# Kernel optimization log

Measured on AMD Instinct MI355X. Metric: run time of the kernel, lower is better.

Reference implementation:

```python
import jax, jax.numpy as jnp
import numpy as np
import math

B, H, S, D = 2, 16, 2048, 128
COEFF = 2.0  # layer_number


def setup_inputs() -> dict:
    key = jax.random.key(0)
    kq, kk, kv = jax.random.split(key, 3)
    return {
        "query_layer": jax.random.normal(kq, (B, H, S, D), dtype=jnp.float32),
        "key_layer": jax.random.normal(kk, (B, H, S, D), dtype=jnp.float32),
        "value_layer": jax.random.normal(kv, (B, H, S, D), dtype=jnp.float32),
    }


def reference(query_layer, key_layer, value_layer):
    b, h, sq, d = query_layer.shape
    sk = key_layer.shape[2]
    norm_factor = math.sqrt(d) * COEFF
    # raw scores [b,h,sq,sk]; divide by sqrt(d)*coeff, cast fp32, multiply by coeff
    scores = jnp.einsum("bhqd,bhkd->bhqk", query_layer, key_layer) / norm_factor
    scores = scores.astype(jnp.float32) * COEFF
    # causal mask (sq == sk path with attention_mask=None)
    causal = jnp.tril(jnp.ones((sq, sk), dtype=bool))
    scores = jnp.where(causal, scores, jnp.float32(-jnp.inf))
    probs = jax.nn.softmax(scores, axis=-1).astype(value_layer.dtype)
    # dropout p=0.0 -> identity
    ctx = jnp.einsum("bhqk,bhkd->bhqd", probs, value_layer)
    # [b,h,sq,d] -> [b,sq,h*d]
    return ctx.transpose(0, 2, 1, 3).reshape(b, sq, h * d)
```

## Files before the change

### kernel.cpp

```cpp
#include <hip/hip_runtime.h>
#include <hip/hip_bf16.h>
#include <math.h>

#define NB 2
#define NH 16
#define NS 2048
#define ND 128

typedef __bf16 bf16x8 __attribute__((ext_vector_type(8)));
typedef __bf16 bf16x4 __attribute__((ext_vector_type(4)));
typedef float f32x4 __attribute__((ext_vector_type(4)));

__global__ __launch_bounds__(256)
void prep(const float* __restrict__ K, const float* __restrict__ V,
          char* __restrict__ Kb, char* __restrict__ Vb)
{
    int g = blockIdx.x * 256 + threadIdx.x;
    if (g < (1 << 20)) {
        const int c8 = g & 15;
        const int row = g >> 4;
        const int s = row & 2047, bh = row >> 11;
        const int jt = s >> 6, r = s & 63;
        const float* src = K + ((size_t)row << 7) + (c8 << 3);
        float4 a = *(const float4*)src;
        float4 c = *(const float4*)(src + 4);
        bf16x8 o;
        o[0]=(__bf16)a.x; o[1]=(__bf16)a.y; o[2]=(__bf16)a.z; o[3]=(__bf16)a.w;
        o[4]=(__bf16)c.x; o[5]=(__bf16)c.y; o[6]=(__bf16)c.z; o[7]=(__bf16)c.w;
        *(bf16x8*)(Kb + (((size_t)(bh*32 + jt)) << 14) + r*256 + ((c8 ^ (r & 7)) << 4)) = o;
    } else {
        g -= (1 << 20);
        const int t   = g >> 10;
        const int off = g & 1023;
        const int d = off >> 3, sl = off & 7;
        const int g8 = sl ^ (d & 7);
        const int bh = t >> 5, jt = t & 31;
        const float* src = V + (((size_t)(bh*2048 + jt*64 + g8*8)) << 7) + d;
        bf16x8 o;
        #pragma unroll
        for (int j = 0; j < 8; ++j) o[j] = (__bf16)src[(size_t)j << 7];
        *(bf16x8*)(Vb + (((size_t)t) << 14) + d*128 + (sl << 4)) = o;
    }
}

__device__ __forceinline__ void gld16(void* lds, const void* gsrc)
{
    __builtin_amdgcn_global_load_lds(
        (const __attribute__((address_space(1))) void*)gsrc,
        (__attribute__((address_space(3))) void*)lds, 16, 0, 0);
}

__global__ __launch_bounds__(256, 2)
void fa_fwd(const float* __restrict__ Qg_, const char* __restrict__ Kb,
            const char* __restrict__ Vb, float* __restrict__ Out)
{
    __shared__ __bf16 Kl[2][8192];
    __shared__ __bf16 Vl[2][8192];
    __shared__ __bf16 Pl[4][1024];

    const int tid  = threadIdx.x;
    const int w    = tid >> 6;
    const int lane = tid & 63;
    const int quad = lane >> 4;
    const int l15  = lane & 15;

    const int pr = blockIdx.x >> 5;
    const int bh = blockIdx.x & 31;
    const int b  = bh >> 4, h = bh & 15;
    const int qtA = 31 - pr, qtB = pr;
    const int ntA = qtA + 1;
    const int total = ntA + qtB + 1;
    const int qA = qtA * 64, qB = qtB * 64;

    const float* Qg = Qg_ + (size_t)bh * NS * ND;
    const char*  Kt = Kb + ((size_t)bh << 19);
    const char*  Vt = Vb + ((size_t)bh << 19);

    const int xo = (l15 & 7) << 4;

    const float CSC = 0.08838834764831845f * 1.4426950408889634f;
    bf16x8 qfA[4], qfB[4], qcur[4];
    {
        const float* qp  = Qg + (size_t)(qA + 16*w + l15) * ND + quad*8;
        const float* qp2 = Qg + (size_t)(qB + 16*w + l15) * ND + quad*8;
        #pragma unroll
        for (int ks = 0; ks < 4; ++ks) {
            float4 a = *(const float4*)(qp + ks*32);
            float4 c = *(const float4*)(qp + ks*32 + 4);
            bf16x8 f;
            f[0]=(__bf16)(a.x*CSC); f[1]=(__bf16)(a.y*CSC); f[2]=(__bf16)(a.z*CSC); f[3]=(__bf16)(a.w*CSC);
            f[4]=(__bf16)(c.x*CSC); f[5]=(__bf16)(c.y*CSC); f[6]=(__bf16)(c.z*CSC); f[7]=(__bf16)(c.w*CSC);
            qfA[ks] = f;
            float4 a2 = *(const float4*)(qp2 + ks*32);
            float4 c2 = *(const float4*)(qp2 + ks*32 + 4);
            bf16x8 f2;
            f2[0]=(__bf16)(a2.x*CSC); f2[1]=(__bf16)(a2.y*CSC); f2[2]=(__bf16)(a2.z*CSC); f2[3]=(__bf16)(a2.w*CSC);
            f2[4]=(__bf16)(c2.x*CSC); f2[5]=(__bf16)(c2.y*CSC); f2[6]=(__bf16)(c2.z*CSC); f2[7]=(__bf16)(c2.w*CSC);
            qfB[ks] = f2;
        }
    }
    #pragma unroll
    for (int ks = 0; ks < 4; ++ks) qcur[ks] = qfA[ks];

    f32x4 O[8];
    #pragma unroll
    for (int dt = 0; dt < 8; ++dt)
        #pragma unroll
        for (int r = 0; r < 4; ++r) O[dt][r] = 0.0f;
    float rs = 0.0f;

    char* const klds0 = (char*)&Kl[0][0];
    char* const vlds0 = (char*)&Vl[0][0];
    char* const Pw    = (char*)&Pl[w][0];

    auto stage = [&](int jt, int buf) {
        const char* kg = Kt + (((size_t)jt) << 14) + w*4096 + lane*16;
        const char* vg = Vt + (((size_t)jt) << 14) + w*4096 + lane*16;
        char* kl = klds0 + buf*16384 + w*4096;
        char* vl = vlds0 + buf*16384 + w*4096;
        #pragma unroll
        for (int i = 0; i < 4; ++i) {
            gld16(kl + i*1024, kg + i*1024);
            gld16(vl + i*1024, vg + i*1024);
        }
    };

    auto flush = [&](int qb) {
        float s1 = rs + __shfl_xor(rs, 16, 64);
        float s2 = s1 + __shfl_xor(s1, 32, 64);
        #pragma unroll
        for (int r = 0; r < 4; ++r) {
            float lsum = __shfl(s2, quad*4 + r, 64);
            float inv = 1.0f / lsum;
            int q = qb + 16*w + quad*4 + r;
            float* op = Out + ((size_t)(b*NS + q)) * (NH*ND) + h*ND + l15;
            #pragma unroll
            for (int dt = 0; dt < 8; ++dt)
                op[dt*16] = O[dt][r] * inv;
        }
    };

    stage(0, 0);
    int cur = 0;

    for (int t = 0; t < total; ++t) {
        const int phase = (t >= ntA);
        const bool diag = (phase ? (t - ntA) == qtB : t == qtA);

        if (t + 1 < total) {
            const int jt2 = (t + 1 >= ntA) ? (t + 1 - ntA) : (t + 1);
            stage(jt2, cur ^ 1);
            asm volatile("s_waitcnt vmcnt(8)" ::: "memory");
        } else {
            asm volatile("s_waitcnt vmcnt(0)" ::: "memory");
        }
        __builtin_amdgcn_s_barrier();
        asm volatile("" ::: "memory");

        if (t == ntA) {
            flush(qA);
            rs = 0.0f;
            #pragma unroll
            for (int dt = 0; dt < 8; ++dt)
                #pragma unroll
                for (int r = 0; r < 4; ++r) O[dt][r] = 0.0f;
            #pragma unroll
            for (int ks = 0; ks < 4; ++ks) qcur[ks] = qfB[ks];
        }

        const char* Kc = klds0 + cur*16384;
        f32x4 Sf[4];
        #pragma unroll
        for (int n = 0; n < 4; ++n)
            #pragma unroll
            for (int r = 0; r < 4; ++r) Sf[n][r] = 0.0f;
        #pragma unroll
        for (int ks = 0; ks < 4; ++ks) {
            bf16x8 kf[4];
            #pragma unroll
            for (int n = 0; n < 4; ++n)
                kf[n] = *(const bf16x8*)(Kc + (n*16 + l15)*256 + ((((ks*4 + quad) << 4)) ^ xo));
            #pragma unroll
            for (int n = 0; n < 4; ++n)
                Sf[n] = __builtin_amdgcn_mfma_f32_16x16x32_bf16(kf[n], qcur[ks], Sf[n], 0, 0, 0);
        }

        #pragma unroll
        for (int n = 0; n < 4; ++n) {
            bf16x4 pk;
            #pragma unroll
            for (int r = 0; r < 4; ++r) {
                float e = exp2f(Sf[n][r]);
                if (diag) {
                    int kvg = n*16 + quad*4 + r;
                    int qg  = 16*w + l15;
                    if (kvg > qg) e = 0.0f;
                }
                pk[r] = (__bf16)e;
                rs += (float)pk[r];
            }
            *(bf16x4*)(Pw + l15*128 + ((((n*2 + (quad >> 1)) << 4)) ^ xo) + ((quad & 1) << 3)) = pk;
        }

        const char* Vc = vlds0 + cur*16384;
        #pragma unroll
        for (int ks = 0; ks < 2; ++ks) {
            bf16x8 pa = *(const bf16x8*)(Pw + l15*128 + ((((ks*4 + quad) << 4)) ^ xo));
            #pragma unroll
            for (int dt = 0; dt < 8; ++dt) {
                bf16x8 vf = *(const bf16x8*)(Vc + (dt*16 + l15)*128 + ((((ks*4 + quad) << 4)) ^ xo));
                O[dt] = __builtin_amdgcn_mfma_f32_16x16x32_bf16(pa, vf, O[dt], 0, 0, 0);
            }
        }

        __syncthreads();
        cur ^= 1;
    }

    flush(qB);
}

extern "C" void kernel_launch(void* const* d_in, const int* in_sizes, int n_in,
                              void* d_out, int out_size, void* d_ws, size_t ws_size,
                              hipStream_t stream) {
    const float* Q = (const float*)d_in[0];
    const float* K = (const float*)d_in[1];
    const float* V = (const float*)d_in[2];
    float* Out = (float*)d_out;
    char* Kb = (char*)d_ws;
    char* Vb = (char*)d_ws + ((size_t)32 << 19);
    prep<<<dim3(8192), dim3(256), 0, stream>>>(K, V, Kb, Vb);
    fa_fwd<<<dim3(512), dim3(256), 0, stream>>>(Q, Kb, Vb, Out);
}
```

Before: 192.2 us.

## Split KV tile across waves, share P in LDS, coalesce V transpose prep

The attention kernel now has each wave own 16 KV rows of the tile and all 64 query rows, holding Q fragments for the whole block in registers. A shared P tile in LDS lets each wave compute two 16-wide slices of the output head dimension, so each wave reads only its own K rows and V columns instead of the full tile. Row sums are combined across waves through LDS at flush time, and MFMA sections get raised scheduling priority. The V prep pass is rewritten to read coalesced float2 rows with one block per tile, and the grid shrinks. This costs more Q registers and an extra barrier per iteration.

```diff
diff --git a/kernel.cpp b/kernel.cpp
--- a/kernel.cpp
+++ b/kernel.cpp
@@ -15,8 +15,8 @@
 void prep(const float* __restrict__ K, const float* __restrict__ V,
           char* __restrict__ Kb, char* __restrict__ Vb)
 {
-    int g = blockIdx.x * 256 + threadIdx.x;
-    if (g < (1 << 20)) {
+    if (blockIdx.x < 4096) {
+        int g = blockIdx.x * 256 + threadIdx.x;
         const int c8 = g & 15;
         const int row = g >> 4;
         const int s = row & 2047, bh = row >> 11;
@@ -29,17 +29,25 @@
         o[4]=(__bf16)c.x; o[5]=(__bf16)c.y; o[6]=(__bf16)c.z; o[7]=(__bf16)c.w;
         *(bf16x8*)(Kb + (((size_t)(bh*32 + jt)) << 14) + r*256 + ((c8 ^ (r & 7)) << 4)) = o;
     } else {
-        g -= (1 << 20);
-        const int t   = g >> 10;
-        const int off = g & 1023;
-        const int d = off >> 3, sl = off & 7;
-        const int g8 = sl ^ (d & 7);
-        const int bh = t >> 5, jt = t & 31;
-        const float* src = V + (((size_t)(bh*2048 + jt*64 + g8*8)) << 7) + d;
-        bf16x8 o;
-        #pragma unroll
-        for (int j = 0; j < 8; ++j) o[j] = (__bf16)src[(size_t)j << 7];
-        *(bf16x8*)(Vb + (((size_t)t) << 14) + d*128 + (sl << 4)) = o;
+        const int T    = blockIdx.x - 4096;
+        const int w2   = threadIdx.x >> 6;
+        const int lane = threadIdx.x & 63;
+        const int d0   = lane << 1;
+        const float2* vbase = (const float2*)V + ((size_t)T << 12);
+        char* ob = Vb + ((size_t)T << 14);
+        #pragma unroll
+        for (int p = 0; p < 2; ++p) {
+            const int kv8 = w2*2 + p;
+            bf16x8 o0, o1;
+            #pragma unroll
+            for (int j = 0; j < 8; ++j) {
+                float2 x = vbase[(size_t)(kv8*8 + j)*64 + lane];
+                o0[j] = (__bf16)x.x;
+                o1[j] = (__bf16)x.y;
+            }
+            *(bf16x8*)(ob + d0*128       + ((kv8 ^ (d0 & 7)) << 4))       = o0;
+            *(bf16x8*)(ob + (d0+1)*128   + ((kv8 ^ ((d0+1) & 7)) << 4))   = o1;
+        }
     }
 }
 
@@ -54,9 +62,10 @@
 void fa_fwd(const float* __restrict__ Qg_, const char* __restrict__ Kb,
             const char* __restrict__ Vb, float* __restrict__ Out)
 {
-    __shared__ __bf16 Kl[2][8192];
-    __shared__ __bf16 Vl[2][8192];
-    __shared__ __bf16 Pl[4][1024];
+    __shared__ char Kl[2][16384];
+    __shared__ char Vl[2][16384];
+    __shared__ char Pl[8192];
+    __shared__ float Rs[4][64];
 
     const int tid  = threadIdx.x;
     const int w    = tid >> 6;
@@ -79,45 +88,40 @@
     const int xo = (l15 & 7) << 4;
 
     const float CSC = 0.08838834764831845f * 1.4426950408889634f;
-    bf16x8 qfA[4], qfB[4], qcur[4];
-    {
-        const float* qp  = Qg + (size_t)(qA + 16*w + l15) * ND + quad*8;
-        const float* qp2 = Qg + (size_t)(qB + 16*w + l15) * ND + quad*8;
-        #pragma unroll
-        for (int ks = 0; ks < 4; ++ks) {
-            float4 a = *(const float4*)(qp + ks*32);
-            float4 c = *(const float4*)(qp + ks*32 + 4);
-            bf16x8 f;
-            f[0]=(__bf16)(a.x*CSC); f[1]=(__bf16)(a.y*CSC); f[2]=(__bf16)(a.z*CSC); f[3]=(__bf16)(a.w*CSC);
-            f[4]=(__bf16)(c.x*CSC); f[5]=(__bf16)(c.y*CSC); f[6]=(__bf16)(c.z*CSC); f[7]=(__bf16)(c.w*CSC);
-            qfA[ks] = f;
-            float4 a2 = *(const float4*)(qp2 + ks*32);
-            float4 c2 = *(const float4*)(qp2 + ks*32 + 4);
-            bf16x8 f2;
-            f2[0]=(__bf16)(a2.x*CSC); f2[1]=(__bf16)(a2.y*CSC); f2[2]=(__bf16)(a2.z*CSC); f2[3]=(__bf16)(a2.w*CSC);
-            f2[4]=(__bf16)(c2.x*CSC); f2[5]=(__bf16)(c2.y*CSC); f2[6]=(__bf16)(c2.z*CSC); f2[7]=(__bf16)(c2.w*CSC);
-            qfB[ks] = f2;
-        }
-    }
+
+    bf16x8 qf[4][4];
+    auto loadQ = [&](int qbase) {
+        #pragma unroll
+        for (int nq = 0; nq < 4; ++nq) {
+            const float* qp = Qg + (size_t)(qbase + nq*16 + l15) * ND + quad*8;
+            #pragma unroll
+            for (int ks = 0; ks < 4; ++ks) {
+                float4 a = *(const float4*)(qp + ks*32);
+                float4 c = *(const float4*)(qp + ks*32 + 4);
+                bf16x8 f;
+                f[0]=(__bf16)(a.x*CSC); f[1]=(__bf16)(a.y*CSC); f[2]=(__bf16)(a.z*CSC); f[3]=(__bf16)(a.w*CSC);
+                f[4]=(__bf16)(c.x*CSC); f[5]=(__bf16)(c.y*CSC); f[6]=(__bf16)(c.z*CSC); f[7]=(__bf16)(c.w*CSC);
+                qf[nq][ks] = f;
+            }
+        }
+    };
+
+    f32x4 O[4][2];
+    float rs[4];
     #pragma unroll
-    for (int ks = 0; ks < 4; ++ks) qcur[ks] = qfA[ks];
-
-    f32x4 O[8];
+    for (int m = 0; m < 4; ++m)
+        #pragma unroll
+        for (int nl = 0; nl < 2; ++nl)
+            #pragma unroll
+            for (int r = 0; r < 4; ++r) O[m][nl][r] = 0.0f;
     #pragma unroll
-    for (int dt = 0; dt < 8; ++dt)
-        #pragma unroll
-        for (int r = 0; r < 4; ++r) O[dt][r] = 0.0f;
-    float rs = 0.0f;
-
-    char* const klds0 = (char*)&Kl[0][0];
-    char* const vlds0 = (char*)&Vl[0][0];
-    char* const Pw    = (char*)&Pl[w][0];
+    for (int nq = 0; nq < 4; ++nq) rs[nq] = 0.0f;
 
     auto stage = [&](int jt, int buf) {
         const char* kg = Kt + (((size_t)jt) << 14) + w*4096 + lane*16;
         const char* vg = Vt + (((size_t)jt) << 14) + w*4096 + lane*16;
-        char* kl = klds0 + buf*16384 + w*4096;
-        char* vl = vlds0 + buf*16384 + w*4096;
+        char* kl = &Kl[buf][0] + w*4096;
+        char* vl = &Vl[buf][0] + w*4096;
         #pragma unroll
         for (int i = 0; i < 4; ++i) {
             gld16(kl + i*1024, kg + i*1024);
@@ -126,20 +130,30 @@
     };
 
     auto flush = [&](int qb) {
-        float s1 = rs + __shfl_xor(rs, 16, 64);
-        float s2 = s1 + __shfl_xor(s1, 32, 64);
-        #pragma unroll
-        for (int r = 0; r < 4; ++r) {
-            float lsum = __shfl(s2, quad*4 + r, 64);
-            float inv = 1.0f / lsum;
-            int q = qb + 16*w + quad*4 + r;
-            float* op = Out + ((size_t)(b*NS + q)) * (NH*ND) + h*ND + l15;
-            #pragma unroll
-            for (int dt = 0; dt < 8; ++dt)
-                op[dt*16] = O[dt][r] * inv;
+        #pragma unroll
+        for (int nq = 0; nq < 4; ++nq) {
+            float v = rs[nq];
+            v += __shfl_xor(v, 16, 64);
+            v += __shfl_xor(v, 32, 64);
+            if (quad == 0) Rs[w][nq*16 + l15] = v;
+        }
+        __syncthreads();
+        #pragma unroll
+        for (int m = 0; m < 4; ++m) {
+            #pragma unroll
+            for (int r = 0; r < 4; ++r) {
+                int qq = m*16 + quad*4 + r;
+                float tt = Rs[0][qq] + Rs[1][qq] + Rs[2][qq] + Rs[3][qq];
+                float inv = 1.0f / tt;
+                int q = qb + qq;
+                float* op = Out + ((size_t)(b*NS + q)) * (NH*ND) + h*ND + l15;
+                op[(2*w)*16]   = O[m][0][r] * inv;
+                op[(2*w+1)*16] = O[m][1][r] * inv;
+            }
         }
     };
 
+    loadQ(qA);
     stage(0, 0);
     int cur = 0;
 
@@ -159,61 +173,75 @@
 
         if (t == ntA) {
             flush(qA);
-            rs = 0.0f;
-            #pragma unroll
-            for (int dt = 0; dt < 8; ++dt)
+            #pragma unroll
+            for (int m = 0; m < 4; ++m)
                 #pragma unroll
-                for (int r = 0; r < 4; ++r) O[dt][r] = 0.0f;
-            #pragma unroll
-            for (int ks = 0; ks < 4; ++ks) qcur[ks] = qfB[ks];
-        }
-
-        const char* Kc = klds0 + cur*16384;
-        f32x4 Sf[4];
-        #pragma unroll
-        for (int n = 0; n < 4; ++n)
-            #pragma unroll
-            for (int r = 0; r < 4; ++r) Sf[n][r] = 0.0f;
-        #pragma unroll
-        for (int ks = 0; ks < 4; ++ks) {
-            bf16x8 kf[4];
-            #pragma unroll
-            for (int n = 0; n < 4; ++n)
-                kf[n] = *(const bf16x8*)(Kc + (n*16 + l15)*256 + ((((ks*4 + quad) << 4)) ^ xo));
-            #pragma unroll
-            for (int n = 0; n < 4; ++n)
-                Sf[n] = __builtin_amdgcn_mfma_f32_16x16x32_bf16(kf[n], qcur[ks], Sf[n], 0, 0, 0);
-        }
-
-        #pragma unroll
-        for (int n = 0; n < 4; ++n) {
+                for (int nl = 0; nl < 2; ++nl)
+                    #pragma unroll
+                    for (int r = 0; r < 4; ++r) O[m][nl][r] = 0.0f;
+            #pragma unroll
+            for (int nq = 0; nq < 4; ++nq) rs[nq] = 0.0f;
+            loadQ(qB);
+        }
+
+        const char* Kc = &Kl[cur][0] + (w*16 + l15)*256;
+        bf16x8 kf[4];
+        #pragma unroll
+        for (int ks = 0; ks < 4; ++ks)
+            kf[ks] = *(const bf16x8*)(Kc + ((((ks*4 + quad) << 4)) ^ xo));
+        f32x4 S[4];
+        #pragma unroll
+        for (int nq = 0; nq < 4; ++nq)
+            #pragma unroll
+            for (int r = 0; r < 4; ++r) S[nq][r] = 0.0f;
+        __builtin_amdgcn_s_setprio(1);
+        #pragma unroll
+        for (int ks = 0; ks < 4; ++ks)
+            #pragma unroll
+            for (int nq = 0; nq < 4; ++nq)
+                S[nq] = __builtin_amdgcn_mfma_f32_16x16x32_bf16(kf[ks], qf[nq][ks], S[nq], 0, 0, 0);
+        __builtin_amdgcn_s_setprio(0);
+
+        const char* Vc = &Vl[cur][0];
+        bf16x8 vfr[2][2];
+        #pragma unroll
+        for (int nl = 0; nl < 2; ++nl)
+            #pragma unroll
+            for (int ks = 0; ks < 2; ++ks)
+                vfr[nl][ks] = *(const bf16x8*)(Vc + ((2*w + nl)*16 + l15)*128 + ((((ks*4 + quad) << 4)) ^ xo));
+
+        #pragma unroll
+        for (int nq = 0; nq < 4; ++nq) {
             bf16x4 pk;
             #pragma unroll
             for (int r = 0; r < 4; ++r) {
-                float e = exp2f(Sf[n][r]);
-                if (diag) {
-                    int kvg = n*16 + quad*4 + r;
-                    int qg  = 16*w + l15;
-                    if (kvg > qg) e = 0.0f;
-                }
+                float e = exp2f(S[nq][r]);
+                if (diag && (w*16 + quad*4 + r > nq*16 + l15)) e = 0.0f;
+                rs[nq] += e;
                 pk[r] = (__bf16)e;
-                rs += (float)pk[r];
-            }
-            *(bf16x4*)(Pw + l15*128 + ((((n*2 + (quad >> 1)) << 4)) ^ xo) + ((quad & 1) << 3)) = pk;
-        }
-
-        const char* Vc = vlds0 + cur*16384;
-        #pragma unroll
-        for (int ks = 0; ks < 2; ++ks) {
-            bf16x8 pa = *(const bf16x8*)(Pw + l15*128 + ((((ks*4 + quad) << 4)) ^ xo));
-            #pragma unroll
-            for (int dt = 0; dt < 8; ++dt) {
-                bf16x8 vf = *(const bf16x8*)(Vc + (dt*16 + l15)*128 + ((((ks*4 + quad) << 4)) ^ xo));
-                O[dt] = __builtin_amdgcn_mfma_f32_16x16x32_bf16(pa, vf, O[dt], 0, 0, 0);
-            }
-        }
-
-        __syncthreads();
+            }
+            *(bf16x4*)(Pl + (nq*16 + l15)*128 + ((((4*w + quad) ^ ((l15 & 7) << 1))) << 3)) = pk;
+        }
+
+        asm volatile("s_waitcnt lgkmcnt(0)" ::: "memory");
+        __builtin_amdgcn_s_barrier();
+        asm volatile("" ::: "memory");
+
+        __builtin_amdgcn_s_setprio(1);
+        #pragma unroll
+        for (int m = 0; m < 4; ++m) {
+            bf16x8 pa0 = *(const bf16x8*)(Pl + (m*16 + l15)*128 + (((quad << 4)) ^ xo));
+            bf16x8 pa1 = *(const bf16x8*)(Pl + (m*16 + l15)*128 + ((((4 + quad) << 4)) ^ xo));
+            O[m][0] = __builtin_amdgcn_mfma_f32_16x16x32_bf16(pa0, vfr[0][0], O[m][0], 0, 0, 0);
+            O[m][1] = __builtin_amdgcn_mfma_f32_16x16x32_bf16(pa0, vfr[1][0], O[m][1], 0, 0, 0);
+            O[m][0] = __builtin_amdgcn_mfma_f32_16x16x32_bf16(pa1, vfr[0][1], O[m][0], 0, 0, 0);
+            O[m][1] = __builtin_amdgcn_mfma_f32_16x16x32_bf16(pa1, vfr[1][1], O[m][1], 0, 0, 0);
+        }
+        __builtin_amdgcn_s_setprio(0);
+
+        asm volatile("" ::: "memory");
+        __builtin_amdgcn_s_barrier();
+        asm volatile("" ::: "memory");
         cur ^= 1;
     }
 
@@ -229,6 +257,6 @@
     float* Out = (float*)d_out;
     char* Kb = (char*)d_ws;
     char* Vb = (char*)d_ws + ((size_t)32 << 19);
-    prep<<<dim3(8192), dim3(256), 0, stream>>>(K, V, Kb, Vb);
+    prep<<<dim3(5120), dim3(256), 0, stream>>>(K, V, Kb, Vb);
     fa_fwd<<<dim3(512), dim3(256), 0, stream>>>(Q, Kb, Vb, Out);
 }
```

Measured after the change: 202.0 us. +5.1%, slower.
